# Performance work log

Measured on AMD Instinct MI355X. Metric: run time of the kernel, lower is better.

Reference implementation:

```python
import jax, jax.numpy as jnp
from jax import lax
import numpy as np

H = W = 2048
C = 3
KSIZE = 2
SIGMA = 2.0
ITERATIONS = 2
RADII = (256.0, 768.0)
# with max_displacement=0 all circle centers coincide, so 'close to any circle'
# reduces to distance^2 < max(radius^2)
SRADII_MAX = max(r ** 2 for r in RADII)
SCLEAN_MAX = max(max(r - KSIZE, 0.0) ** 2 for r in RADII)


def _gaussian_blur(x, sigma):
    """skimage.filters.gaussian equivalent: separable gaussian, truncate=4.0,
    mode='nearest' (edge padding), channel_axis=-1 (no blur across channels)."""
    radius = int(4.0 * sigma + 0.5)
    t = np.arange(-radius, radius + 1, dtype=np.float32)
    k = np.exp(-0.5 * (t / sigma) ** 2)
    k = (k / k.sum()).astype(np.float32)
    for axis in (0, 1):
        pad = [(0, 0)] * x.ndim
        pad[axis] = (radius, radius)
        xp = jnp.pad(x, pad, mode='edge')
        n = x.shape[axis]
        acc = jnp.zeros_like(x)
        for j in range(k.shape[0]):
            acc = acc + k[j] * lax.slice_in_dim(xp, j, j + n, axis=axis)
        x = acc
    return x


def _glass_forward(img, offsets):
    r = KSIZE
    Hv = H - 2 * r + 1  # loop range(r, H-r+1) -> H-2r+1 rows
    Wv = W - 2 * r + 1
    HWtot = H * W
    # original quirk: cx = shape[0]//2 compared against column index w,
    # cy = shape[1]//2 against row index h; identical for a square image.
    cx = H // 2
    cy = W // 2
    ys = jnp.arange(r, H - r + 1)
    xs = jnp.arange(r, W - r + 1)
    HH, WW = jnp.meshgrid(ys, xs, indexing='ij')  # (Hv, Wv)
    d2 = (cx - WW) ** 2 + (cy - HH) ** 2
    swap_mask = (d2 >= SRADII_MAX).reshape(-1)  # swap only OUTSIDE all circles
    local = ((HH - r) * Wv + (WW - r)).reshape(-1)  # raster order within loop
    lin = (HH * W + WW).reshape(-1)

    # Every read in the original swap loop comes from array_orig (never
    # updated), so the final value of each pixel equals array_orig[source]
    # where source is determined by the LAST write targeting that pixel.
    # Each loop step emits two ordered writes:
    #   array[h, w]   = orig[h_, w_]   (order = 2*raster)
    #   array[h_, w_] = orig[h, w]    (order = 2*raster + 1)
    # We replay this exactly with a scatter-max over write order.
    writes = []
    for i in range(ITERATIONS):
        dh = offsets[i, :, :, 0]
        dw = offsets[i, :, :, 1]
        lin_ = ((HH + dh) * W + (WW + dw)).reshape(-1)
        base = i * 2 * Hv * Wv
        o1 = base + 2 * local
        o2 = o1 + 1
        writes.append((lin, lin_, o1))
        writes.append((lin_, lin, o2))

    win = jnp.full((HWtot,), -1, jnp.int32)
    for tgt, src_idx, order in writes:
        win = win.at[tgt].max(jnp.where(swap_mask, order, -1))
    src = jnp.full((HWtot,), -1, jnp.int32)
    for tgt, src_idx, order in writes:
        hit = swap_mask & (order == win[tgt])
        src = src.at[tgt].max(jnp.where(hit, src_idx, -1))

    orig_flat = img.reshape(HWtot, C)
    gathered = orig_flat[jnp.maximum(src, 0)]
    swapped = jnp.where((src >= 0)[:, None], gathered, orig_flat).reshape(H, W, C)

    blurred = jnp.clip(_gaussian_blur(swapped / 255.0, SIGMA), 0.0, 1.0) * 255.0

    # restore original pixels close to the shrunken (clean) circles
    clean = d2 < SCLEAN_MAX  # (Hv, Wv)
    clean_full = jnp.zeros((H, W), bool).at[r:H - r + 1, r:W - r + 1].set(clean)
    return jnp.where(clean_full[:, :, None], img, blurred)


def setup_inputs() -> dict:
    key = jax.random.key(0)
    k1, k2 = jax.random.split(key)
    img = jax.random.uniform(k1, (H, W, C), jnp.float32) * 255.0
    offsets = jax.random.randint(
        k2, (ITERATIONS, H - 2 * KSIZE + 1, W - 2 * KSIZE + 1, 2),
        -KSIZE, KSIZE, dtype=jnp.int32)
    return {"img": img, "offsets": offsets}


def reference(img, offsets):
    return _glass_forward(img, offsets)
```

## Files before the change

### kernel.cpp

```cpp
#include <hip/hip_runtime.h>
#include <hip/hip_fp16.h>

#define Hh 2048
#define Ww 2048
#define HW (2048 * 2048)
constexpr int REG = 2045;
constexpr int RBASE = 2 * 2045 * 2045;
constexpr int SWAP_D2 = 589824;
constexpr int CLEAN_D2 = 586756;
constexpr int SKIP_D2 = 569000;

__device__ __constant__ float GK[17] = {
    6.691628e-05f, 4.363490e-04f, 2.215963e-03f, 8.764304e-03f,
    2.699596e-02f, 6.475994e-02f, 1.209875e-01f, 1.760358e-01f,
    1.9947466e-01f, 1.760358e-01f, 1.209875e-01f, 6.475994e-02f,
    2.699596e-02f, 8.764304e-03f, 2.215963e-03f, 4.363490e-04f,
    6.691628e-05f};

__device__ __forceinline__ int clampi(int v, int lo, int hi) {
  return v < lo ? lo : (v > hi ? hi : v);
}

constexpr int TX = 32, TY = 8;
constexpr int HX = TX + 3, HY = TY + 3;

__global__ __launch_bounds__(256) void swap_gather(
    const float* __restrict__ img, const int* __restrict__ off,
    __half* __restrict__ A) {
  __shared__ unsigned sh[HY * HX];
  __shared__ __align__(16) float simg[12 * 108];
  int x0 = blockIdx.x * TX, y0 = blockIdx.y * TY;
  int tx = threadIdx.x & 31, ty = threadIdx.x >> 5;
  int px = x0 + tx, py = y0 + ty;
  int plin = py * Ww + px;

  int bxx = max(abs(1024 - x0), abs(1024 - (x0 + TX - 1)));
  int bxy = max(abs(1024 - y0), abs(1024 - (y0 + TY - 1)));
  if (bxx * bxx + bxy * bxy < SKIP_D2) return;

  float r, g, b;
  int mxx = max(abs(1024 - (x0 - 1)), abs(1024 - (x0 + TX + 1)));
  int mxy = max(abs(1024 - (y0 - 1)), abs(1024 - (y0 + TY + 1)));
  if (mxx * mxx + mxy * mxy >= SWAP_D2) {
    for (int e = threadIdx.x; e < HY * HX; e += 256) {
      int ly = e / HX, lx = e - ly * HX;
      int qy = y0 - 1 + ly, qx = x0 - 1 + lx;
      unsigned v = 0xFFFFFFFFu;
      int dcx = 1024 - qx, dcy = 1024 - qy;
      if (qy >= 2 && qy <= 2046 && qx >= 2 && qx <= 2046 &&
          dcx * dcx + dcy * dcy >= SWAP_D2) {
        int base = ((qy - 2) * REG + (qx - 2)) * 2;
        const int2 a0 = *(const int2*)&off[base];
        const int2 a1 = *(const int2*)&off[RBASE + base];
        v = (unsigned)(a0.y + 2) | ((unsigned)(a0.x + 2) << 8) |
            ((unsigned)(a1.y + 2) << 16) | ((unsigned)(a1.x + 2) << 24);
      }
      sh[e] = v;
    }
    if (x0 >= 2 && x0 <= 2013) {
      for (int e = threadIdx.x; e < 648; e += 256) {
        int rr = e / 54, c2 = e - rr * 54;
        int qy = clampi(y0 - 2 + rr, 0, 2047);
        *(float2*)&simg[rr * 108 + 2 * c2] =
            *(const float2*)&img[(size_t)qy * 6144 + (size_t)(x0 - 2) * 3 +
                                 2 * c2];
      }
    } else {
      for (int e = threadIdx.x; e < 1296; e += 256) {
        int rr = e / 108, c3 = e - rr * 108;
        int col = c3 / 3, ch = c3 - col * 3;
        int qy = clampi(y0 - 2 + rr, 0, 2047);
        int qx = clampi(x0 - 2 + col, 0, 2047);
        simg[e] = img[((size_t)qy * Ww + qx) * 3 + ch];
      }
    }
    __syncthreads();

    unsigned w[4][4];
#pragma unroll
    for (int dyi = 0; dyi < 4; ++dyi)
#pragma unroll
      for (int dxi = 0; dxi < 4; ++dxi)
        w[dyi][dxi] = sh[(ty + dyi) * HX + (tx + dxi)];

    int loff = 0;
#define CANDC(dyi, dxi) ((unsigned)((1 - (dxi)) + 2) | ((unsigned)((1 - (dyi)) + 2) << 8))
#define LOFFC(dyi, dxi) (-(1 - (dyi)) * 36 - (1 - (dxi)))
#define CAND0(dyi, dxi) \
  if ((w[dyi][dxi] & 0xFFFFu) == CANDC(dyi, dxi)) loff = LOFFC(dyi, dxi);
#define CAND1(dyi, dxi) \
  if ((w[dyi][dxi] >> 16) == CANDC(dyi, dxi)) loff = LOFFC(dyi, dxi);

    CAND0(0, 0) CAND0(0, 1) CAND0(0, 2) CAND0(0, 3)
    CAND0(1, 0) CAND0(1, 1) CAND0(1, 2) CAND0(1, 3)
    CAND0(2, 0) CAND0(2, 1) CAND0(2, 2) CAND0(2, 3)
    CAND0(3, 0) CAND0(3, 1) CAND0(3, 2) CAND0(3, 3)
    CAND1(0, 0) CAND1(0, 1) CAND1(0, 2) CAND1(0, 3)
    CAND1(1, 0)
    {
      unsigned wc = w[1][1];
      if ((wc >> 24) != 0xFFu) {
        int dh1 = (int)((wc >> 24) & 0xFFu) - 2;
        int dw1 = (int)((wc >> 16) & 0xFFu) - 2;
        loff = dh1 * 36 + dw1;
      }
    }
    CAND1(1, 1) CAND1(1, 2) CAND1(1, 3)
    CAND1(2, 0) CAND1(2, 1) CAND1(2, 2) CAND1(2, 3)
    CAND1(3, 0) CAND1(3, 1) CAND1(3, 2) CAND1(3, 3)
#undef CANDC
#undef LOFFC
#undef CAND0
#undef CAND1

    int L = ((ty + 2) * 36 + (tx + 2) + loff) * 3;
    r = simg[L + 0];
    g = simg[L + 1];
    b = simg[L + 2];
  } else {
    r = img[(size_t)plin * 3 + 0];
    g = img[(size_t)plin * 3 + 1];
    b = img[(size_t)plin * 3 + 2];
  }
  A[plin] = __float2half(r);
  A[HW + plin] = __float2half(g);
  A[2 * HW + plin] = __float2half(b);
}

constexpr int BTW = 128, BTH = 32;
constexpr int SW = BTW + 16;
constexpr int SH = BTH + 16;

__global__ __launch_bounds__(256) void blur_compose(
    const __half* __restrict__ A, const float* __restrict__ img,
    float* __restrict__ out) {
  int lin = blockIdx.x;
  int swz = (lin & 7) * 128 + (lin >> 3);
  int tyb = swz & 63, txb = swz >> 6;
  int x0 = txb * BTW, y0 = tyb * BTH;
  int tid = threadIdx.x;

  int mxx = max(abs(1024 - x0), abs(1024 - (x0 + BTW - 1)));
  int mxy = max(abs(1024 - y0), abs(1024 - (y0 + BTH - 1)));
  if (mxx * mxx + mxy * mxy < CLEAN_D2) {
    const float4* ip = (const float4*)(img + ((size_t)y0 * Ww + x0) * 3);
    float4* op = (float4*)(out + ((size_t)y0 * Ww + x0) * 3);
    for (int e = tid; e < 3072; e += 256) {
      int rr = e / 96, c4 = e - rr * 96;
      op[(size_t)rr * 1536 + c4] = ip[(size_t)rr * 1536 + c4];
    }
    return;
  }

  __shared__ __align__(16) __half S[SH * SW];
  __shared__ __align__(8) __half V[BTH * SW];

  bool xin = (x0 >= 8) && (x0 + SW - 8 <= Ww);

  for (int c = 0; c < 3; ++c) {
    const __half* Ap = A + (size_t)c * HW;
    __syncthreads();
    if (xin) {
      for (int e = tid; e < SH * 18; e += 256) {
        int rr = e / 18, ch = e - rr * 18;
        int ys = clampi(y0 - 8 + rr, 0, Hh - 1);
        *(uint4*)&S[rr * SW + ch * 8] =
            *(const uint4*)&Ap[(size_t)ys * Ww + (x0 - 8) + ch * 8];
      }
    } else {
      for (int e = tid; e < SH * SW; e += 256) {
        int rr = e / SW, j = e - rr * SW;
        int ys = clampi(y0 - 8 + rr, 0, Hh - 1);
        int xs = clampi(x0 - 8 + j, 0, Ww - 1);
        S[e] = Ap[(size_t)ys * Ww + xs];
      }
    }
    __syncthreads();
    for (int e = tid; e < BTH * 72; e += 256) {
      int rr = e / 72, p = e - rr * 72;
      float s0 = 0.f, s1 = 0.f;
#pragma unroll
      for (int t = 0; t < 17; ++t) {
        float2 v = __half22float2(*(const __half2*)&S[(rr + t) * SW + 2 * p]);
        s0 += GK[t] * v.x;
        s1 += GK[t] * v.y;
      }
      *(__half2*)&V[rr * SW + 2 * p] = __float22half2_rn(make_float2(s0, s1));
    }
    __syncthreads();
    for (int e = tid; e < BTH * 64; e += 256) {
      int rr = e >> 6, xh = e & 63;
      int x = 2 * xh;
      float f[18];
#pragma unroll
      for (int t = 0; t < 9; ++t) {
        float2 v = __half22float2(*(const __half2*)&V[rr * SW + x + 2 * t]);
        f[2 * t] = v.x;
        f[2 * t + 1] = v.y;
      }
      float s0 = 0.f, s1 = 0.f;
#pragma unroll
      for (int t = 0; t < 17; ++t) {
        s0 += GK[t] * f[t];
        s1 += GK[t] * f[t + 1];
      }
      int y = y0 + rr;
      int xg = x0 + x;
      int dy = 1024 - y;
#pragma unroll
      for (int u = 0; u < 2; ++u) {
        int xu = xg + u;
        int dx = 1024 - xu;
        bool clean = (xu >= 2 && xu <= 2046 && y >= 2 && y <= 2046 &&
                      dx * dx + dy * dy < CLEAN_D2);
        int p3 = (y * Ww + xu) * 3 + c;
        float v = u ? s1 : s0;
        v = v < 0.f ? 0.f : (v > 255.f ? 255.f : v);
        if (clean)
          out[p3] = img[p3];
        else
          out[p3] = v;
      }
    }
  }
}

extern "C" void kernel_launch(void* const* d_in, const int* in_sizes, int n_in,
                              void* d_out, int out_size, void* d_ws,
                              size_t ws_size, hipStream_t stream) {
  const float* img = (const float*)d_in[0];
  const int* off = (const int*)d_in[1];
  float* out = (float*)d_out;

  __half* A = (__half*)d_ws;

  swap_gather<<<dim3(Ww / TX, Hh / TY), 256, 0, stream>>>(img, off, A);
  blur_compose<<<1024, 256, 0, stream>>>(A, img, out);
}
```

Measured before the change: 203.3 us.

## Buffer blurred channels in registers and write interleaved RGB with vector stores

The blur kernel now keeps the blurred results for all three channels in registers and writes each output pixel pair as contiguous float2 stores after the channel loop. Previously each channel pass issued separate stride-3 scalar stores. The tile height is halved, with the grid and block swizzle doubled to match. The redundant barrier at the top of the channel loop is removed. The change targets uncoalesced output writes, at the cost of extra live registers (24 floats per thread).

New measurement: 194.6 us. 1.04x faster.

```diff
diff --git a/kernel.cpp b/kernel.cpp
--- a/kernel.cpp
+++ b/kernel.cpp
@@ -127,7 +127,7 @@
   A[2 * HW + plin] = __float2half(b);
 }
 
-constexpr int BTW = 128, BTH = 32;
+constexpr int BTW = 128, BTH = 16;
 constexpr int SW = BTW + 16;
 constexpr int SH = BTH + 16;
 
@@ -135,8 +135,8 @@
     const __half* __restrict__ A, const float* __restrict__ img,
     float* __restrict__ out) {
   int lin = blockIdx.x;
-  int swz = (lin & 7) * 128 + (lin >> 3);
-  int tyb = swz & 63, txb = swz >> 6;
+  int swz = (lin & 7) * 256 + (lin >> 3);
+  int tyb = swz & 127, txb = swz >> 7;
   int x0 = txb * BTW, y0 = tyb * BTH;
   int tid = threadIdx.x;
 
@@ -145,7 +145,7 @@
   if (mxx * mxx + mxy * mxy < CLEAN_D2) {
     const float4* ip = (const float4*)(img + ((size_t)y0 * Ww + x0) * 3);
     float4* op = (float4*)(out + ((size_t)y0 * Ww + x0) * 3);
-    for (int e = tid; e < 3072; e += 256) {
+    for (int e = tid; e < 1536; e += 256) {
       int rr = e / 96, c4 = e - rr * 96;
       op[(size_t)rr * 1536 + c4] = ip[(size_t)rr * 1536 + c4];
     }
@@ -157,9 +157,10 @@
 
   bool xin = (x0 >= 8) && (x0 + SW - 8 <= Ww);
 
+  float br[3][4][2];
+
   for (int c = 0; c < 3; ++c) {
     const __half* Ap = A + (size_t)c * HW;
-    __syncthreads();
     if (xin) {
       for (int e = tid; e < SH * 18; e += 256) {
         int rr = e / 18, ch = e - rr * 18;
@@ -188,9 +189,10 @@
       *(__half2*)&V[rr * SW + 2 * p] = __float22half2_rn(make_float2(s0, s1));
     }
     __syncthreads();
-    for (int e = tid; e < BTH * 64; e += 256) {
-      int rr = e >> 6, xh = e & 63;
-      int x = 2 * xh;
+#pragma unroll
+    for (int k = 0; k < 4; ++k) {
+      int e = tid + (k << 8);
+      int rr = e >> 6, x = (e & 63) * 2;
       float f[18];
 #pragma unroll
       for (int t = 0; t < 9; ++t) {
@@ -204,24 +206,44 @@
         s0 += GK[t] * f[t];
         s1 += GK[t] * f[t + 1];
       }
-      int y = y0 + rr;
-      int xg = x0 + x;
-      int dy = 1024 - y;
-#pragma unroll
-      for (int u = 0; u < 2; ++u) {
-        int xu = xg + u;
-        int dx = 1024 - xu;
-        bool clean = (xu >= 2 && xu <= 2046 && y >= 2 && y <= 2046 &&
-                      dx * dx + dy * dy < CLEAN_D2);
-        int p3 = (y * Ww + xu) * 3 + c;
-        float v = u ? s1 : s0;
-        v = v < 0.f ? 0.f : (v > 255.f ? 255.f : v);
-        if (clean)
-          out[p3] = img[p3];
-        else
-          out[p3] = v;
-      }
-    }
+      br[c][k][0] = s0;
+      br[c][k][1] = s1;
+    }
+  }
+
+#pragma unroll
+  for (int k = 0; k < 4; ++k) {
+    int e = tid + (k << 8);
+    int rr = e >> 6, xh = e & 63;
+    int y = y0 + rr;
+    int xg = x0 + 2 * xh;
+    int dy = 1024 - y;
+    int dy2 = dy * dy;
+    float px[6];
+#pragma unroll
+    for (int u = 0; u < 2; ++u) {
+      int xu = xg + u;
+      int dx = 1024 - xu;
+      bool clean = (xu >= 2 && xu <= 2046 && y >= 2 && y <= 2046 &&
+                    dx * dx + dy2 < CLEAN_D2);
+      int p3 = (y * Ww + xu) * 3;
+      if (clean) {
+        px[3 * u + 0] = img[p3 + 0];
+        px[3 * u + 1] = img[p3 + 1];
+        px[3 * u + 2] = img[p3 + 2];
+      } else {
+#pragma unroll
+        for (int cc = 0; cc < 3; ++cc) {
+          float v = br[cc][k][u];
+          v = v < 0.f ? 0.f : (v > 255.f ? 255.f : v);
+          px[3 * u + cc] = v;
+        }
+      }
+    }
+    float* ob = out + (size_t)(y * Ww + xg) * 3;
+    *(float2*)&ob[0] = make_float2(px[0], px[1]);
+    *(float2*)&ob[2] = make_float2(px[2], px[3]);
+    *(float2*)&ob[4] = make_float2(px[4], px[5]);
   }
 }
 
@@ -235,5 +257,5 @@
   __half* A = (__half*)d_ws;
 
   swap_gather<<<dim3(Ww / TX, Hh / TY), 256, 0, stream>>>(img, off, A);
-  blur_compose<<<1024, 256, 0, stream>>>(A, img, out);
-}
+  blur_compose<<<2048, 256, 0, stream>>>(A, img, out);
+}
```
